# Kernel tuning notes

Hardware: AMD Instinct MI355X
Metric: run time of the kernel (lower is better)

Reference implementation:

```python
import jax, jax.numpy as jnp
import numpy as np

N, E = 50000, 800000
IN_DIM, H, D = 128, 8, 16  # num_heads=8, out_dim(per head)=16


def setup_inputs() -> dict:
    key = jax.random.key(0)
    ks = jax.random.split(key, 9)
    s = 1.0 / np.sqrt(IN_DIM)
    return {
        "h": jax.random.normal(ks[0], (N, IN_DIM), dtype=jnp.float32),
        "Wq": jax.random.normal(ks[1], (IN_DIM, H * D), dtype=jnp.float32) * s,
        "bq": jnp.zeros((H * D,), dtype=jnp.float32),
        "Wk": jax.random.normal(ks[2], (IN_DIM, H * D), dtype=jnp.float32) * s,
        "bk": jnp.zeros((H * D,), dtype=jnp.float32),
        "Wv": jax.random.normal(ks[3], (IN_DIM, H * D), dtype=jnp.float32) * s,
        "bv": jnp.zeros((H * D,), dtype=jnp.float32),
        "src": jax.random.randint(ks[4], (E,), 0, N, dtype=jnp.int32),
        "dst": jax.random.randint(ks[5], (E,), 0, N, dtype=jnp.int32),
    }


def reference(h, Wq, bq, Wk, bk, Wv, bv, src, dst):
    n = h.shape[0]
    Q = (h @ Wq + bq).reshape(n, H, D)
    K = (h @ Wk + bk).reshape(n, H, D)
    V = (h @ Wv + bv).reshape(n, H, D)
    # edge score: u_mul_v(K, Q).sum(-1) / sqrt(D), clamped to [-5, 5]
    score = jnp.einsum("ehd,ehd->eh", K[src], Q[dst]) / jnp.sqrt(
        jnp.asarray(D, h.dtype)
    )  # [E, H]
    score = jnp.clip(score, -5.0, 5.0)
    # edge_softmax over edges sharing the same destination node
    smax = jax.ops.segment_max(score, dst, num_segments=n)  # [N, H]
    ex = jnp.exp(score - smax[dst])
    denom = jax.ops.segment_sum(ex, dst, num_segments=n)  # [N, H]
    a = ex / denom[dst]  # [E, H]
    # u_mul_e(V, a) then sum to destination
    m = V[src] * a[:, :, None]  # [E, H, D]
    wV = jax.ops.segment_sum(m, dst, num_segments=n)  # [N, H, D]
    return wV.reshape(n, H * D)
```

## Files before the change

### kernel.cpp

```cpp
#include <hip/hip_runtime.h>
#include <hip/hip_bf16.h>


typedef short short8 __attribute__((ext_vector_type(8)));
typedef float f32x4 __attribute__((ext_vector_type(4)));

__device__ __forceinline__ unsigned pack_bf16(float a, float b) {
    unsigned ua = __float_as_uint(a), ub = __float_as_uint(b);
    ua += 0x7fffu + ((ua >> 16) & 1u);
    ub += 0x7fffu + ((ub >> 16) & 1u);
    return (ua >> 16) | (ub & 0xffff0000u);
}

#define ULO(u) __uint_as_float((u) << 16)
#define UHI(u) __uint_as_float((u) & 0xffff0000u)

__global__ __launch_bounds__(256) void prep_all(
    const float* __restrict__ W0, const float* __restrict__ W1,
    const float* __restrict__ W2, unsigned char* __restrict__ WTb,
    int* __restrict__ counts, int n)
{
    const int b = blockIdx.x;
    if (b < 24) {
        const int w   = b >> 3;
        const int idx = (b & 7) * 256 + threadIdx.x;
        const float* W = (w == 0) ? W0 : (w == 1) ? W1 : W2;
        unsigned char* wt = WTb + w * 32768;
        const int kp = idx >> 5;
        const int c4 = (idx & 31) * 4;
        const float* Wp = W + (size_t)(2 * kp) * 128 + c4;
        float4 wa = *(const float4*)Wp;
        float4 wb = *(const float4*)(Wp + 128);
        float a0[4] = {wa.x, wa.y, wa.z, wa.w};
        float a1[4] = {wb.x, wb.y, wb.z, wb.w};
#pragma unroll
        for (int i = 0; i < 4; ++i) {
            const int col = c4 + i;
            *(unsigned*)(wt + col * 256 + ((4 * kp) ^ ((col & 7) << 4))) =
                pack_bf16(a0[i], a1[i]);
        }
    } else {
        const int i = (b - 24) * 256 + threadIdx.x;
        if (i < n) counts[i] = 0;
    }
}

__global__ void hist_rank(const int* __restrict__ dst, int* __restrict__ counts,
                          int* __restrict__ rank, int e) {
    int i = blockIdx.x * blockDim.x + threadIdx.x;
    if (i < e) rank[i] = atomicAdd(&counts[dst[i]], 1);
}

__global__ void scan_block_sums(const int* __restrict__ counts, int* __restrict__ bsums, int nelem) {
    __shared__ int red[4];
    int i = blockIdx.x * 256 + threadIdx.x;
    int v = (i < nelem) ? counts[i] : 0;
#pragma unroll
    for (int o = 32; o > 0; o >>= 1) v += __shfl_down(v, o, 64);
    if ((threadIdx.x & 63) == 0) red[threadIdx.x >> 6] = v;
    __syncthreads();
    if (threadIdx.x == 0) bsums[blockIdx.x] = red[0] + red[1] + red[2] + red[3];
}

__global__ void scan_final2(const int* __restrict__ counts, const int* __restrict__ bsums,
                            int* __restrict__ offsets, int nelem, int e) {
    __shared__ int tmp[256];
    __shared__ int red[4];
    const int t = threadIdx.x;

    int pre = (t < blockIdx.x) ? bsums[t] : 0;
#pragma unroll
    for (int o = 32; o > 0; o >>= 1) pre += __shfl_down(pre, o, 64);
    if ((t & 63) == 0) red[t >> 6] = pre;
    __syncthreads();
    const int base = red[0] + red[1] + red[2] + red[3];

    const int i = blockIdx.x * 256 + t;
    int v = (i < nelem) ? counts[i] : 0;
    tmp[t] = v;
    __syncthreads();
    for (int o = 1; o < 256; o <<= 1) {
        int u = (t >= o) ? tmp[t - o] : 0;
        __syncthreads();
        tmp[t] += u;
        __syncthreads();
    }
    if (i < nelem) offsets[i] = base + tmp[t] - v;
    if (i == nelem) offsets[nelem] = e;
}

__global__ void fill_kernel(const int* __restrict__ src, const int* __restrict__ dst,
                            const int* __restrict__ rank, const int* __restrict__ offsets,
                            int* __restrict__ srcSorted, int e) {
    int i = blockIdx.x * blockDim.x + threadIdx.x;
    if (i < e) srcSorted[offsets[dst[i]] + rank[i]] = src[i];
}

__global__ __launch_bounds__(512) void qkv_gemm(
    const float* __restrict__ h, const unsigned char* __restrict__ WTb,
    const float* __restrict__ b0, const float* __restrict__ b1,
    const float* __restrict__ b2,
    unsigned* __restrict__ qb, unsigned* __restrict__ kb, unsigned* __restrict__ vb,
    int n)
{
    __shared__ __align__(16) unsigned char lds[32768];
    const int tid  = threadIdx.x;
    const int row0 = blockIdx.x * 64;

    for (int idx = tid; idx < 2048; idx += 512) {
        const int row = idx >> 5;
        const int c4  = (idx & 31) * 4;
        float4 v = make_float4(0.f, 0.f, 0.f, 0.f);
        if (row0 + row < n) v = *(const float4*)(h + (size_t)(row0 + row) * 128 + c4);
        *(uint2*)(lds + row * 256 + ((c4 * 2) ^ ((row & 7) << 4))) =
            make_uint2(pack_bf16(v.x, v.y), pack_bf16(v.z, v.w));
    }

    const float* bs[3] = {b0, b1, b2};
    unsigned* planes[3] = {qb, kb, vb};

    const int lane = tid & 63, wave = tid >> 6;
    const int wr = wave >> 2, wc = wave & 3;
    const int lr = lane & 15, lg = lane >> 4;

    __syncthreads();

    short8 af[2][4];
#pragma unroll
    for (int mt = 0; mt < 2; ++mt)
#pragma unroll
        for (int ks = 0; ks < 4; ++ks) {
            const int row = wr * 32 + mt * 16 + lr;
            const int kbyte = ks * 64 + lg * 16;
            af[mt][ks] = *(const short8*)(lds + row * 256 + (kbyte ^ ((row & 7) << 4)));
        }

    for (int w = 0; w < 3; ++w) {
        short8 bf[2][4];
#pragma unroll
        for (int nt = 0; nt < 2; ++nt)
#pragma unroll
            for (int ks = 0; ks < 4; ++ks) {
                const int col = wc * 32 + nt * 16 + lr;
                const int kbyte = ks * 64 + lg * 16;
                bf[nt][ks] = *(const short8*)(
                    WTb + w * 32768 + col * 256 + (kbyte ^ ((col & 7) << 4)));
            }

        f32x4 acc[2][2];
#pragma unroll
        for (int nt = 0; nt < 2; ++nt) {
            const float bv = bs[w][wc * 32 + nt * 16 + lr];
            acc[0][nt] = (f32x4){bv, bv, bv, bv};
            acc[1][nt] = (f32x4){bv, bv, bv, bv};
        }
#pragma unroll
        for (int ks = 0; ks < 4; ++ks)
#pragma unroll
            for (int mt = 0; mt < 2; ++mt)
#pragma unroll
                for (int nt = 0; nt < 2; ++nt)
                    acc[mt][nt] = __builtin_amdgcn_mfma_f32_16x16x32_bf16(
                        af[mt][ks], bf[nt][ks], acc[mt][nt], 0, 0, 0);

        __syncthreads();
        {
            unsigned* epi = (unsigned*)(lds + 16384);
#pragma unroll
            for (int mt = 0; mt < 2; ++mt)
#pragma unroll
                for (int nt = 0; nt < 2; ++nt) {
                    const int col = wc * 32 + nt * 16 + lr;
#pragma unroll
                    for (int r = 0; r < 4; ++r) {
                        const int row = wr * 32 + mt * 16 + lg * 4 + r;
                        const float v  = acc[mt][nt][r];
                        const float vn = __shfl_xor(v, 1);
                        if (!(lane & 1)) epi[row * 64 + (col >> 1)] = pack_bf16(v, vn);
                    }
                }
        }
        __syncthreads();
        {
            const uint4* s = (const uint4*)(lds + 16384);
            uint4* d = (uint4*)(planes[w] + (size_t)row0 * 64);
            d[tid]       = s[tid];
            d[tid + 512] = s[tid + 512];
        }
    }
}

__global__ __launch_bounds__(256) void mha_node(
    const unsigned* __restrict__ Qb, const uint2* __restrict__ Kb2,
    const uint2* __restrict__ Vb2,
    const int* __restrict__ offsets, const int* __restrict__ srcSorted,
    float* __restrict__ out, int n)
{
    const int lane = threadIdx.x & 63;
    const int node = (blockIdx.x * blockDim.x + threadIdx.x) >> 6;
    if (node >= n) return;
    const int half = lane >> 5;
    const int l5   = lane & 31;

    const float QS = 0.25f * 1.44269504089f;
    const float CL = 5.f * 1.44269504089f;

    const uint2 qu = *(const uint2*)(Qb + (size_t)node * 64 + 2 * l5);
    const float q0 = ULO(qu.x) * QS, q1 = UHI(qu.x) * QS;
    const float q2 = ULO(qu.y) * QS, q3 = UHI(qu.y) * QS;

    const int beg = offsets[node], end = offsets[node + 1];
    float a0 = 0.f, a1 = 0.f, a2 = 0.f, a3 = 0.f, lsum = 0.f;

#define PAIR_COMPUTE(ku, vu, val)                                       \
    {                                                                   \
        float prod = ULO((ku).x) * q0;                                  \
        prod = fmaf(UHI((ku).x), q1, prod);                             \
        prod = fmaf(ULO((ku).y), q2, prod);                             \
        prod = fmaf(UHI((ku).y), q3, prod);                             \
        prod += __shfl_xor(prod, 1);                                    \
        prod += __shfl_xor(prod, 2);                                    \
        float sc = fminf(CL, fmaxf(-CL, prod));                         \
        float p = (val) ? exp2f(sc) : 0.f;                              \
        lsum += p;                                                      \
        a0 = fmaf(p, ULO((vu).x), a0);                                  \
        a1 = fmaf(p, UHI((vu).x), a1);                                  \
        a2 = fmaf(p, ULO((vu).y), a2);                                  \
        a3 = fmaf(p, UHI((vu).y), a3);                                  \
    }

    for (int j0 = beg; j0 < end; j0 += 64) {
        const int rem = end - j0;
        const int cnt = rem < 64 ? rem : 64;
        int myS = (lane < cnt) ? srcSorted[j0 + lane] : 0;

        int t = 0;
        for (; t + 8 <= cnt; t += 8) {
            uint2 ku[4], vu[4];
#pragma unroll
            for (int u = 0; u < 4; ++u) {
                int s = __shfl(myS, t + 2 * u + half);
                ku[u] = Kb2[(size_t)s * 32 + l5];
                vu[u] = Vb2[(size_t)s * 32 + l5];
            }
#pragma unroll
            for (int u = 0; u < 4; ++u) PAIR_COMPUTE(ku[u], vu[u], true);
        }
        for (; t < cnt; t += 2) {
            const int ei = t + half;
            const bool val = ei < cnt;
            int s = __shfl(myS, val ? ei : cnt - 1);
            uint2 ku0 = Kb2[(size_t)s * 32 + l5];
            uint2 vu0 = Vb2[(size_t)s * 32 + l5];
            PAIR_COMPUTE(ku0, vu0, val);
        }
    }

    lsum += __shfl_xor(lsum, 32);
    a0 += __shfl_xor(a0, 32);
    a1 += __shfl_xor(a1, 32);
    a2 += __shfl_xor(a2, 32);
    a3 += __shfl_xor(a3, 32);

    if (half == 0) {
        const float inv = (lsum > 0.f) ? 1.f / lsum : 0.f;
        *(float4*)(out + (size_t)node * 128 + 4 * l5) =
            make_float4(a0 * inv, a1 * inv, a2 * inv, a3 * inv);
    }
}

extern "C" void kernel_launch(void* const* d_in, const int* in_sizes, int n_in,
                              void* d_out, int out_size, void* d_ws, size_t ws_size,
                              hipStream_t stream) {
    const float* h  = (const float*)d_in[0];
    const float* Wq = (const float*)d_in[1];
    const float* bq = (const float*)d_in[2];
    const float* Wk = (const float*)d_in[3];
    const float* bk = (const float*)d_in[4];
    const float* Wv = (const float*)d_in[5];
    const float* bv = (const float*)d_in[6];
    const int*   src = (const int*)d_in[7];
    const int*   dst = (const int*)d_in[8];
    float* out = (float*)d_out;

    const int n = in_sizes[0] / 128;
    const int e = in_sizes[7];
    const int nblk = (n + 63) / 64;
    const int npad = nblk * 64;
    const int nb = (n + 255) / 256;

    char* ws = (char*)d_ws;
    size_t off = 0;
    auto alloc = [&](size_t bytes) {
        char* p = ws + off;
        off = (off + bytes + 255) & ~(size_t)255;
        return p;
    };
    unsigned char* WTb = (unsigned char*)alloc(3 * 32768);
    unsigned* Qb       = (unsigned*)alloc((size_t)npad * 64 * 4);
    unsigned* Kb       = (unsigned*)alloc((size_t)npad * 64 * 4);
    unsigned* Vb       = (unsigned*)alloc((size_t)npad * 64 * 4);
    int* counts        = (int*)alloc((size_t)n * sizeof(int));
    int* offsets       = (int*)alloc((size_t)(n + 1) * sizeof(int));
    int* rank          = (int*)alloc((size_t)e * sizeof(int));
    int* bsums         = (int*)alloc((size_t)nb * sizeof(int));
    int* srcSorted     = (int*)alloc((size_t)e * sizeof(int));
    (void)ws_size; (void)n_in; (void)out_size;

    prep_all<<<24 + nb, 256, 0, stream>>>(Wq, Wk, Wv, WTb, counts, n);
    hist_rank<<<(e + 255) / 256, 256, 0, stream>>>(dst, counts, rank, e);
    scan_block_sums<<<nb, 256, 0, stream>>>(counts, bsums, n);
    scan_final2<<<nb, 256, 0, stream>>>(counts, bsums, offsets, n, e);
    fill_kernel<<<(e + 255) / 256, 256, 0, stream>>>(src, dst, rank, offsets, srcSorted, e);
    qkv_gemm<<<nblk, 512, 0, stream>>>(h, WTb, bq, bk, bv, Qb, Kb, Vb, n);
    mha_node<<<((size_t)n * 64 + 255) / 256, 256, 0, stream>>>(
        Qb, (const uint2*)Kb, (const uint2*)Vb, offsets, srcSorted, out, n);
}
```

Measured before the change: 142.2 us.

## Fuse CSR build kernels into one cooperative kernel with grid syncs

Merges the five CSR construction kernels (weight prep plus count zeroing, histogram/rank, block sums, scan, fill) into a single cooperative kernel of 1024 blocks that uses grid-wide syncs between phases. This removes four kernel launch gaps and their launch overhead. In exchange, grid.sync barriers are added, edge loops become grid-stride with fewer blocks, and the kernel assumes nb is at most 256 and that 1024 blocks can be co-resident.

```diff
diff --git a/kernel.cpp b/kernel.cpp
--- a/kernel.cpp
+++ b/kernel.cpp
@@ -1,5 +1,8 @@
 #include <hip/hip_runtime.h>
 #include <hip/hip_bf16.h>
+#include <hip/hip_cooperative_groups.h>
+
+namespace cg = cooperative_groups;
 
 
 typedef short short8 __attribute__((ext_vector_type(8)));
@@ -15,15 +18,23 @@
 #define ULO(u) __uint_as_float((u) << 16)
 #define UHI(u) __uint_as_float((u) & 0xffff0000u)
 
-__global__ __launch_bounds__(256) void prep_all(
+__global__ __launch_bounds__(256) void csr_coop(
     const float* __restrict__ W0, const float* __restrict__ W1,
     const float* __restrict__ W2, unsigned char* __restrict__ WTb,
-    int* __restrict__ counts, int n)
+    const int* __restrict__ src, const int* __restrict__ dst,
+    int* __restrict__ counts, int* __restrict__ rank,
+    int* __restrict__ bsums, int* __restrict__ offsets,
+    int* __restrict__ srcSorted, int n, int e, int nb)
 {
-    const int b = blockIdx.x;
+    cg::grid_group grid = cg::this_grid();
+    __shared__ int tmp[256];
+    __shared__ int red[4];
+    const int b = blockIdx.x, t = threadIdx.x;
+    const int gstride = (int)gridDim.x * 256;
+
     if (b < 24) {
         const int w   = b >> 3;
-        const int idx = (b & 7) * 256 + threadIdx.x;
+        const int idx = (b & 7) * 256 + t;
         const float* W = (w == 0) ? W0 : (w == 1) ? W1 : W2;
         unsigned char* wt = WTb + w * 32768;
         const int kp = idx >> 5;
@@ -40,60 +51,51 @@
                 pack_bf16(a0[i], a1[i]);
         }
     } else {
-        const int i = (b - 24) * 256 + threadIdx.x;
-        if (i < n) counts[i] = 0;
-    }
-}
-
-__global__ void hist_rank(const int* __restrict__ dst, int* __restrict__ counts,
-                          int* __restrict__ rank, int e) {
-    int i = blockIdx.x * blockDim.x + threadIdx.x;
-    if (i < e) rank[i] = atomicAdd(&counts[dst[i]], 1);
-}
-
-__global__ void scan_block_sums(const int* __restrict__ counts, int* __restrict__ bsums, int nelem) {
-    __shared__ int red[4];
-    int i = blockIdx.x * 256 + threadIdx.x;
-    int v = (i < nelem) ? counts[i] : 0;
-#pragma unroll
-    for (int o = 32; o > 0; o >>= 1) v += __shfl_down(v, o, 64);
-    if ((threadIdx.x & 63) == 0) red[threadIdx.x >> 6] = v;
-    __syncthreads();
-    if (threadIdx.x == 0) bsums[blockIdx.x] = red[0] + red[1] + red[2] + red[3];
-}
-
-__global__ void scan_final2(const int* __restrict__ counts, const int* __restrict__ bsums,
-                            int* __restrict__ offsets, int nelem, int e) {
-    __shared__ int tmp[256];
-    __shared__ int red[4];
-    const int t = threadIdx.x;
-
-    int pre = (t < blockIdx.x) ? bsums[t] : 0;
-#pragma unroll
-    for (int o = 32; o > 0; o >>= 1) pre += __shfl_down(pre, o, 64);
-    if ((t & 63) == 0) red[t >> 6] = pre;
-    __syncthreads();
-    const int base = red[0] + red[1] + red[2] + red[3];
-
-    const int i = blockIdx.x * 256 + t;
-    int v = (i < nelem) ? counts[i] : 0;
-    tmp[t] = v;
-    __syncthreads();
-    for (int o = 1; o < 256; o <<= 1) {
-        int u = (t >= o) ? tmp[t - o] : 0;
-        __syncthreads();
-        tmp[t] += u;
-        __syncthreads();
-    }
-    if (i < nelem) offsets[i] = base + tmp[t] - v;
-    if (i == nelem) offsets[nelem] = e;
-}
-
-__global__ void fill_kernel(const int* __restrict__ src, const int* __restrict__ dst,
-                            const int* __restrict__ rank, const int* __restrict__ offsets,
-                            int* __restrict__ srcSorted, int e) {
-    int i = blockIdx.x * blockDim.x + threadIdx.x;
-    if (i < e) srcSorted[offsets[dst[i]] + rank[i]] = src[i];
+        for (int i = (b - 24) * 256 + t; i < n; i += ((int)gridDim.x - 24) * 256)
+            counts[i] = 0;
+    }
+    grid.sync();
+
+    for (int i = b * 256 + t; i < e; i += gstride)
+        rank[i] = atomicAdd(&counts[dst[i]], 1);
+    grid.sync();
+
+    if (b < nb) {
+        const int i = b * 256 + t;
+        int v = (i < n) ? counts[i] : 0;
+#pragma unroll
+        for (int o = 32; o > 0; o >>= 1) v += __shfl_down(v, o, 64);
+        if ((t & 63) == 0) red[t >> 6] = v;
+        __syncthreads();
+        if (t == 0) bsums[b] = red[0] + red[1] + red[2] + red[3];
+    }
+    grid.sync();
+
+    if (b < nb) {
+        int pre = (t < b) ? bsums[t] : 0;
+#pragma unroll
+        for (int o = 32; o > 0; o >>= 1) pre += __shfl_down(pre, o, 64);
+        if ((t & 63) == 0) red[t >> 6] = pre;
+        __syncthreads();
+        const int base = red[0] + red[1] + red[2] + red[3];
+
+        const int i = b * 256 + t;
+        int v = (i < n) ? counts[i] : 0;
+        tmp[t] = v;
+        __syncthreads();
+        for (int o = 1; o < 256; o <<= 1) {
+            int u = (t >= o) ? tmp[t - o] : 0;
+            __syncthreads();
+            tmp[t] += u;
+            __syncthreads();
+        }
+        if (i < n) offsets[i] = base + tmp[t] - v;
+        if (i == n) offsets[n] = e;
+    }
+    grid.sync();
+
+    for (int i = b * 256 + t; i < e; i += gstride)
+        srcSorted[offsets[dst[i]] + rank[i]] = src[i];
 }
 
 __global__ __launch_bounds__(512) void qkv_gemm(
@@ -283,11 +285,11 @@
     const int*   dst = (const int*)d_in[8];
     float* out = (float*)d_out;
 
-    const int n = in_sizes[0] / 128;
-    const int e = in_sizes[7];
+    int n = in_sizes[0] / 128;
+    int e = in_sizes[7];
     const int nblk = (n + 63) / 64;
     const int npad = nblk * 64;
-    const int nb = (n + 255) / 256;
+    int nb = (n + 255) / 256;
 
     char* ws = (char*)d_ws;
     size_t off = 0;
@@ -307,11 +309,15 @@
     int* srcSorted     = (int*)alloc((size_t)e * sizeof(int));
     (void)ws_size; (void)n_in; (void)out_size;
 
-    prep_all<<<24 + nb, 256, 0, stream>>>(Wq, Wk, Wv, WTb, counts, n);
-    hist_rank<<<(e + 255) / 256, 256, 0, stream>>>(dst, counts, rank, e);
-    scan_block_sums<<<nb, 256, 0, stream>>>(counts, bsums, n);
-    scan_final2<<<nb, 256, 0, stream>>>(counts, bsums, offsets, n, e);
-    fill_kernel<<<(e + 255) / 256, 256, 0, stream>>>(src, dst, rank, offsets, srcSorted, e);
+    void* args[] = {
+        (void*)&Wq, (void*)&Wk, (void*)&Wv, (void*)&WTb,
+        (void*)&src, (void*)&dst,
+        (void*)&counts, (void*)&rank, (void*)&bsums, (void*)&offsets,
+        (void*)&srcSorted, (void*)&n, (void*)&e, (void*)&nb
+    };
+    hipLaunchCooperativeKernel((const void*)csr_coop, dim3(1024), dim3(256),
+                               args, 0, stream);
+
     qkv_gemm<<<nblk, 512, 0, stream>>>(h, WTb, bq, bk, bv, Qb, Kb, Vb, n);
     mha_node<<<((size_t)n * 64 + 255) / 256, 256, 0, stream>>>(
         Qb, (const uint2*)Kb, (const uint2*)Vb, offsets, srcSorted, out, n);
```

Result: slower. 511.8 us (+260.0%).
